# Performance work log

Hardware: AMD Instinct MI355X
Metric: run time of the kernel (lower is better)

Reference implementation:

```python
import jax, jax.numpy as jnp
import numpy as np

USER_COUNT = 100000
ITEM_COUNT = 50000
LATENT = 64
N_LAYERS = 3
NEG_SLOPE = 0.2


def _xavier(key, shape):
    fan_in, fan_out = shape[-2], shape[-1]
    lim = jnp.sqrt(6.0 / (fan_in + fan_out))
    return jax.random.uniform(key, shape, jnp.float32, -lim, lim)


def setup_inputs() -> dict:
    key = jax.random.key(0)
    ks = jax.random.split(key, 20)
    E = 2400000
    edge_index = jax.random.randint(ks[0], (2, E), 0, USER_COUNT + ITEM_COUNT, dtype=jnp.int64)
    user = jax.random.randint(ks[1], (4096,), 0, USER_COUNT, dtype=jnp.int64)
    item = jax.random.randint(ks[2], (4096,), 0, ITEM_COUNT, dtype=jnp.int64)
    inp = {"user": user, "item": item, "edge_index": edge_index}
    # online encoder params
    inp["user_emb_o"] = _xavier(ks[3], (USER_COUNT, LATENT))
    inp["item_emb_o"] = _xavier(ks[4], (ITEM_COUNT, LATENT))
    inp["W_o"] = _xavier(ks[5], (N_LAYERS, LATENT, LATENT))
    inp["att_src_o"] = _xavier(ks[6], (N_LAYERS, 1, LATENT))[:, 0, :]
    inp["att_dst_o"] = _xavier(ks[7], (N_LAYERS, 1, LATENT))[:, 0, :]
    inp["bias_o"] = jnp.zeros((N_LAYERS, LATENT), jnp.float32)
    # target encoder params (momentum copy; frozen in torch)
    inp["user_emb_t"] = _xavier(ks[8], (USER_COUNT, LATENT))
    inp["item_emb_t"] = _xavier(ks[9], (ITEM_COUNT, LATENT))
    inp["W_t"] = _xavier(ks[10], (N_LAYERS, LATENT, LATENT))
    inp["att_src_t"] = _xavier(ks[11], (N_LAYERS, 1, LATENT))[:, 0, :]
    inp["att_dst_t"] = _xavier(ks[12], (N_LAYERS, 1, LATENT))[:, 0, :]
    inp["bias_t"] = jnp.zeros((N_LAYERS, LATENT), jnp.float32)
    # predictor Linear(latent, latent)
    inp["pred_W"] = _xavier(ks[13], (LATENT, LATENT))
    inp["pred_b"] = jnp.zeros((LATENT,), jnp.float32)
    return inp


def _gat_conv(x, src, dst, n_nodes, W, a_src, a_dst, b):
    # PyG GATConv, heads=1, concat=True, add_self_loops handled by caller.
    h = x @ W                                   # [N, F]
    e = jax.nn.leaky_relu(jnp.take(h @ a_src, src) + jnp.take(h @ a_dst, dst), NEG_SLOPE)  # [E]
    m = jax.ops.segment_max(e, dst, num_segments=n_nodes)
    m = jnp.where(jnp.isfinite(m), m, 0.0)
    ex = jnp.exp(e - jnp.take(m, dst))
    den = jax.ops.segment_sum(ex, dst, num_segments=n_nodes)
    alpha = ex / jnp.take(den, dst)             # softmax over incoming edges per dst
    msg = alpha[:, None] * jnp.take(h, src, axis=0)  # [E, F]
    return jax.ops.segment_sum(msg, dst, num_segments=n_nodes) + b


def _encode(user_emb, item_emb, W, a_src, a_dst, bias, src, dst):
    x = jnp.concatenate([user_emb, item_emb], axis=0)  # [N, F]
    n_nodes = x.shape[0]
    for l in range(N_LAYERS):
        x = _gat_conv(x, src, dst, n_nodes, W[l], a_src[l], a_dst[l], bias[l])
    return x[:user_emb.shape[0]], x[user_emb.shape[0]:]


def reference(user_emb_o, item_emb_o, W_o, att_src_o, att_dst_o, bias_o,
              user_emb_t, item_emb_t, W_t, att_src_t, att_dst_t, bias_t,
              pred_W, pred_b, user, item, edge_index):
    n_nodes = user_emb_o.shape[0] + item_emb_o.shape[0]
    loops = jnp.arange(n_nodes, dtype=edge_index.dtype)
    src = jnp.concatenate([edge_index[0], loops])  # add self loops (PyG default)
    dst = jnp.concatenate([edge_index[1], loops])
    u_all_o, i_all_o = _encode(user_emb_o, item_emb_o, W_o, att_src_o, att_dst_o, bias_o, src, dst)
    u_all_t, i_all_t = _encode(user_emb_t, item_emb_t, W_t, att_src_t, att_dst_t, bias_t, src, dst)
    u_online = jnp.take(u_all_o, user, axis=0)
    i_online = jnp.take(i_all_o, item, axis=0)
    u_target = jnp.take(u_all_t, user, axis=0)
    i_target = jnp.take(i_all_t, item, axis=0)
    return (u_online @ pred_W.T + pred_b, u_target, i_online @ pred_W.T + pred_b, i_target)
```

## Files before the change

### kernel.cpp

```cpp
#include <hip/hip_runtime.h>
#include <math.h>
#include <stdint.h>

#define LAT 64
#define SLICE 16384

static inline int cdiv(int a, int b) { return (a + b - 1) / b; }

__global__ void k_count(const int* __restrict__ dst_arr, int E, int N, int* __restrict__ cnt) {
    int e = blockIdx.x * blockDim.x + threadIdx.x;
    int ET = E + N;
    if (e < ET) {
        int d = (e < E) ? dst_arr[e] : (e - E);
        atomicAdd(&cnt[d], 1);
    }
}

__global__ void k_scan1(const int* __restrict__ cnt, int N, int* __restrict__ out, int* __restrict__ blk_sums) {
    __shared__ int sdata[256];
    int t = threadIdx.x, b = blockIdx.x;
    int base = b * 1024 + t * 4;
    int v[4];
    int s = 0;
#pragma unroll
    for (int u = 0; u < 4; u++) { int i = base + u; v[u] = (i < N) ? cnt[i] : 0; s += v[u]; }
    sdata[t] = s; __syncthreads();
    for (int off = 1; off < 256; off <<= 1) {
        int x = (t >= off) ? sdata[t - off] : 0;
        __syncthreads();
        sdata[t] += x;
        __syncthreads();
    }
    int run = sdata[t] - s;
#pragma unroll
    for (int u = 0; u < 4; u++) { int i = base + u; if (i < N) out[i] = run; run += v[u]; }
    if (t == 255) blk_sums[b] = sdata[255];
}

__global__ void k_scan2(int* __restrict__ blk_sums, int NB) {
    __shared__ int sdata[256];
    int t = threadIdx.x;
    int v = (t < NB) ? blk_sums[t] : 0;
    sdata[t] = v; __syncthreads();
    for (int off = 1; off < 256; off <<= 1) {
        int x = (t >= off) ? sdata[t - off] : 0;
        __syncthreads();
        sdata[t] += x;
        __syncthreads();
    }
    if (t < NB) blk_sums[t] = sdata[t] - v;
}

__global__ void k_scan3(int* __restrict__ row_ptr, const int* __restrict__ blk_offs, int N, int ET) {
    int t = threadIdx.x, b = blockIdx.x;
    int base = b * 1024 + t * 4;
    int off = blk_offs[b];
#pragma unroll
    for (int u = 0; u < 4; u++) { int i = base + u; if (i < N) row_ptr[i] += off; }
    if (b == 0 && t == 0) row_ptr[N] = ET;
}

__global__ void k_scatter(const int* __restrict__ src_arr, const int* __restrict__ dst_arr, int E, int N,
                          const int* __restrict__ row_ptr, int* __restrict__ cnt, int* __restrict__ csr_src) {
    int ET = E + N;
    int slice = blockIdx.x >> 3;
    int range = blockIdx.x & 7;
    int rsz = (N + 7) >> 3;
    int lo = range * rsz;
    int hi = lo + rsz; if (hi > N) hi = N;
    int base = slice * SLICE;
    int end = base + SLICE; if (end > ET) end = ET;
    for (int e = base + threadIdx.x; e < end; e += 256) {
        int s, d;
        if (e < E) { s = src_arr[e]; d = dst_arr[e]; }
        else { s = e - E; d = e - E; }
        if (d >= lo && d < hi) {
            int pos = atomicAdd(&cnt[d], 1);
            csr_src[row_ptr[d] + pos] = s;
        }
    }
}


__global__ __launch_bounds__(256) void k_gemm2(const float* __restrict__ x,
                                               const float* __restrict__ ue, const float* __restrict__ ie, int NU,
                                               const float* __restrict__ W,
                                               const float* __restrict__ att_s, const float* __restrict__ att_d,
                                               float* __restrict__ h2e, float* __restrict__ asp, float* __restrict__ adp,
                                               int N) {
    __shared__ float sW[64 * 64];
    __shared__ float sX[128 * 65];
    __shared__ float sAs[64], sAd[64];
    int t = threadIdx.x;
    int row0 = blockIdx.x * 128;
    {
        const float4* Wv = (const float4*)W;
        float4* sWv = (float4*)sW;
#pragma unroll
        for (int u = 0; u < 4; u++) sWv[t + 256 * u] = Wv[t + 256 * u];
    }
    if (t < 64) { sAs[t] = att_s[t]; sAd[t] = att_d[t]; }
    {
#pragma unroll
        for (int u = 0; u < 8; u++) {
            int idx = t + 256 * u;
            int r = idx >> 4, c4 = idx & 15;
            int grow = row0 + r;
            float4 v = make_float4(0.f, 0.f, 0.f, 0.f);
            if (grow < N) {
                const float* base = x ? (x + (size_t)grow * 64)
                                      : (grow < NU ? ue + (size_t)grow * 64 : ie + (size_t)(grow - NU) * 64);
                v = ((const float4*)base)[c4];
            }
            int cc = c4 * 4;
            sX[r * 65 + cc] = v.x; sX[r * 65 + cc + 1] = v.y; sX[r * 65 + cc + 2] = v.z; sX[r * 65 + cc + 3] = v.w;
        }
    }
    __syncthreads();
    int rl = t >> 2;
    int g = t & 3;
    int c0 = g * 16;
    int rA = rl * 2, rB = rA + 1;
    float accA[16], accB[16];
#pragma unroll
    for (int j = 0; j < 16; j++) { accA[j] = 0.f; accB[j] = 0.f; }
    for (int k = 0; k < 64; k++) {
        float xa = sX[rA * 65 + k];
        float xb = sX[rB * 65 + k];
        const float4* wr = (const float4*)&sW[k * 64 + c0];
        float4 w0 = wr[0], w1 = wr[1], w2 = wr[2], w3 = wr[3];
        accA[0] += xa * w0.x; accA[1] += xa * w0.y; accA[2] += xa * w0.z; accA[3] += xa * w0.w;
        accA[4] += xa * w1.x; accA[5] += xa * w1.y; accA[6] += xa * w1.z; accA[7] += xa * w1.w;
        accA[8] += xa * w2.x; accA[9] += xa * w2.y; accA[10] += xa * w2.z; accA[11] += xa * w2.w;
        accA[12] += xa * w3.x; accA[13] += xa * w3.y; accA[14] += xa * w3.z; accA[15] += xa * w3.w;
        accB[0] += xb * w0.x; accB[1] += xb * w0.y; accB[2] += xb * w0.z; accB[3] += xb * w0.w;
        accB[4] += xb * w1.x; accB[5] += xb * w1.y; accB[6] += xb * w1.z; accB[7] += xb * w1.w;
        accB[8] += xb * w2.x; accB[9] += xb * w2.y; accB[10] += xb * w2.z; accB[11] += xb * w2.w;
        accB[12] += xb * w3.x; accB[13] += xb * w3.y; accB[14] += xb * w3.z; accB[15] += xb * w3.w;
    }
    float sA = 0.f, dA = 0.f, sB = 0.f, dB = 0.f;
#pragma unroll
    for (int j = 0; j < 16; j++) {
        sA += accA[j] * sAs[c0 + j]; dA += accA[j] * sAd[c0 + j];
        sB += accB[j] * sAs[c0 + j]; dB += accB[j] * sAd[c0 + j];
    }
    sA += __shfl_xor(sA, 1); sA += __shfl_xor(sA, 2);
    dA += __shfl_xor(dA, 1); dA += __shfl_xor(dA, 2);
    sB += __shfl_xor(sB, 1); sB += __shfl_xor(sB, 2);
    dB += __shfl_xor(dB, 1); dB += __shfl_xor(dB, 2);
    int rowA = row0 + rA, rowB = row0 + rB;
    if (rowA < N) {
        if (g == 0) { asp[(size_t)rowA * 2] = sA; adp[(size_t)rowA * 2] = dA; }
        float4* hv = (float4*)&h2e[(size_t)rowA * 128 + c0];
        hv[0] = make_float4(accA[0], accA[1], accA[2], accA[3]);
        hv[1] = make_float4(accA[4], accA[5], accA[6], accA[7]);
        hv[2] = make_float4(accA[8], accA[9], accA[10], accA[11]);
        hv[3] = make_float4(accA[12], accA[13], accA[14], accA[15]);
    }
    if (rowB < N) {
        if (g == 0) { asp[(size_t)rowB * 2] = sB; adp[(size_t)rowB * 2] = dB; }
        float4* hv = (float4*)&h2e[(size_t)rowB * 128 + c0];
        hv[0] = make_float4(accB[0], accB[1], accB[2], accB[3]);
        hv[1] = make_float4(accB[4], accB[5], accB[6], accB[7]);
        hv[2] = make_float4(accB[8], accB[9], accB[10], accB[11]);
        hv[3] = make_float4(accB[12], accB[13], accB[14], accB[15]);
    }
}

__global__ __launch_bounds__(256) void k_agg2(const float* __restrict__ h2,
                                              const int* __restrict__ row_ptr, const int* __restrict__ csr_src,
                                              const float2* __restrict__ asv, const float2* __restrict__ adv,
                                              const float* __restrict__ bias_o, const float* __restrict__ bias_t,
                                              float* __restrict__ xo, float* __restrict__ xt, int N,
                                              const int* __restrict__ selu, const int* __restrict__ seli,
                                              int nSel, int nSelU, int NU,
                                              float* __restrict__ selxo, float* __restrict__ outT_u,
                                              float* __restrict__ outT_i) {
    int wid = threadIdx.x >> 6, lane = threadIdx.x & 63;
    int r = blockIdx.x * 4 + wid;
    int d;
    float *po, *pt;
    if (selu) {
        if (r >= nSel) return;
        if (r < nSelU) { d = selu[r]; pt = outT_u + (size_t)r * 64; }
        else { int rr = r - nSelU; d = seli[rr] + NU; pt = outT_i + (size_t)rr * 64; }
        po = selxo + (size_t)r * 64;
    } else {
        if (r >= N) return;
        d = r;
        po = xo + (size_t)d * 64;
        pt = xt + (size_t)d * 64;
    }
    int s0 = row_ptr[d], s1 = row_ptr[d + 1];
    float2 advv = adv[d];
    int j0 = s0 + lane;
    int sv0 = 0; float eo0 = -1e30f, et0 = -1e30f;
    if (j0 < s1) {
        sv0 = csr_src[j0];
        float2 a2 = asv[sv0];
        float eo = a2.x + advv.x; eo0 = (eo > 0.f) ? eo : 0.2f * eo;
        float et = a2.y + advv.y; et0 = (et > 0.f) ? et : 0.2f * et;
    }
    float mo = eo0, mt = et0;
    for (int j = j0 + 64; j < s1; j += 64) {
        float2 a2 = asv[csr_src[j]];
        float eo = a2.x + advv.x; eo = (eo > 0.f) ? eo : 0.2f * eo; mo = fmaxf(mo, eo);
        float et = a2.y + advv.y; et = (et > 0.f) ? et : 0.2f * et; mt = fmaxf(mt, et);
    }
#pragma unroll
    for (int o = 32; o; o >>= 1) { mo = fmaxf(mo, __shfl_xor(mo, o)); mt = fmaxf(mt, __shfl_xor(mt, o)); }
    float exo0 = (j0 < s1) ? expf(eo0 - mo) : 0.f;
    float ext0 = (j0 < s1) ? expf(et0 - mt) : 0.f;
    float so = exo0, st = ext0;
    for (int j = j0 + 64; j < s1; j += 64) {
        float2 a2 = asv[csr_src[j]];
        float eo = a2.x + advv.x; eo = (eo > 0.f) ? eo : 0.2f * eo; so += expf(eo - mo);
        float et = a2.y + advv.y; et = (et > 0.f) ? et : 0.2f * et; st += expf(et - mt);
    }
#pragma unroll
    for (int o = 32; o; o >>= 1) { so += __shfl_xor(so, o); st += __shfl_xor(st, o); }
    float invo = 1.f / so, invt = 1.f / st;
    exo0 *= invo; ext0 *= invt;
    int sub = lane >> 4, c4 = lane & 15;
    float4 ao = make_float4(0.f, 0.f, 0.f, 0.f);
    float4 at4 = make_float4(0.f, 0.f, 0.f, 0.f);
    for (int cb = s0; cb < s1; cb += 64) {
        int sv; float wo, wt;
        if (cb == s0) { sv = sv0; wo = exo0; wt = ext0; }
        else {
            int jj = cb + lane; sv = 0; wo = 0.f; wt = 0.f;
            if (jj < s1) {
                sv = csr_src[jj];
                float2 a2 = asv[sv];
                float eo = a2.x + advv.x; eo = (eo > 0.f) ? eo : 0.2f * eo; wo = expf(eo - mo) * invo;
                float et = a2.y + advv.y; et = (et > 0.f) ? et : 0.2f * et; wt = expf(et - mt) * invt;
            }
        }
        int c = s1 - cb; if (c > 64) c = 64;
        for (int q = 0; q < c; q += 4) {
            int il = q + sub;
            int s = __shfl(sv, il);
            float o_ = __shfl(wo, il);
            float t_ = __shfl(wt, il);
            const float* hb = h2 + (size_t)s * 128 + (c4 << 2);
            float4 ho = *(const float4*)hb;
            float4 ht = *(const float4*)(hb + 64);
            ao.x += o_ * ho.x; ao.y += o_ * ho.y; ao.z += o_ * ho.z; ao.w += o_ * ho.w;
            at4.x += t_ * ht.x; at4.y += t_ * ht.y; at4.z += t_ * ht.z; at4.w += t_ * ht.w;
        }
    }
#pragma unroll
    for (int o = 16; o <= 32; o <<= 1) {
        ao.x += __shfl_xor(ao.x, o); ao.y += __shfl_xor(ao.y, o);
        ao.z += __shfl_xor(ao.z, o); ao.w += __shfl_xor(ao.w, o);
        at4.x += __shfl_xor(at4.x, o); at4.y += __shfl_xor(at4.y, o);
        at4.z += __shfl_xor(at4.z, o); at4.w += __shfl_xor(at4.w, o);
    }
    if (lane < 16) {
        float4 bo = ((const float4*)bias_o)[c4];
        ao.x += bo.x; ao.y += bo.y; ao.z += bo.z; ao.w += bo.w;
        ((float4*)po)[c4] = ao;
        float4 bt = ((const float4*)bias_t)[c4];
        at4.x += bt.x; at4.y += bt.y; at4.z += bt.z; at4.w += bt.w;
        ((float4*)pt)[c4] = at4;
    }
}

__global__ __launch_bounds__(256) void k_gemm(const float* __restrict__ x,
                                              const float* __restrict__ ue, const float* __restrict__ ie, int NU,
                                              const float* __restrict__ W,
                                              const float* __restrict__ att_s, const float* __restrict__ att_d,
                                              float* __restrict__ h, float* __restrict__ as_, float* __restrict__ ad_,
                                              int N) {
    __shared__ float sW[64 * 64];
    __shared__ float sX[128 * 65];
    __shared__ float sAs[64], sAd[64];
    int t = threadIdx.x;
    int row0 = blockIdx.x * 128;
    {
        const float4* Wv = (const float4*)W;
        float4* sWv = (float4*)sW;
#pragma unroll
        for (int u = 0; u < 4; u++) sWv[t + 256 * u] = Wv[t + 256 * u];
    }
    if (t < 64) { sAs[t] = att_s[t]; sAd[t] = att_d[t]; }
    {
#pragma unroll
        for (int u = 0; u < 8; u++) {
            int idx = t + 256 * u;
            int r = idx >> 4, c4 = idx & 15;
            int grow = row0 + r;
            float4 v = make_float4(0.f, 0.f, 0.f, 0.f);
            if (grow < N) {
                const float* base = x ? (x + (size_t)grow * 64)
                                      : (grow < NU ? ue + (size_t)grow * 64 : ie + (size_t)(grow - NU) * 64);
                v = ((const float4*)base)[c4];
            }
            int cc = c4 * 4;
            sX[r * 65 + cc] = v.x; sX[r * 65 + cc + 1] = v.y; sX[r * 65 + cc + 2] = v.z; sX[r * 65 + cc + 3] = v.w;
        }
    }
    __syncthreads();
    int rl = t >> 2;
    int g = t & 3;
    int c0 = g * 16;
    int rA = rl * 2, rB = rA + 1;
    float accA[16], accB[16];
#pragma unroll
    for (int j = 0; j < 16; j++) { accA[j] = 0.f; accB[j] = 0.f; }
    for (int k = 0; k < 64; k++) {
        float xa = sX[rA * 65 + k];
        float xb = sX[rB * 65 + k];
        const float4* wr = (const float4*)&sW[k * 64 + c0];
        float4 w0 = wr[0], w1 = wr[1], w2 = wr[2], w3 = wr[3];
        accA[0] += xa * w0.x; accA[1] += xa * w0.y; accA[2] += xa * w0.z; accA[3] += xa * w0.w;
        accA[4] += xa * w1.x; accA[5] += xa * w1.y; accA[6] += xa * w1.z; accA[7] += xa * w1.w;
        accA[8] += xa * w2.x; accA[9] += xa * w2.y; accA[10] += xa * w2.z; accA[11] += xa * w2.w;
        accA[12] += xa * w3.x; accA[13] += xa * w3.y; accA[14] += xa * w3.z; accA[15] += xa * w3.w;
        accB[0] += xb * w0.x; accB[1] += xb * w0.y; accB[2] += xb * w0.z; accB[3] += xb * w0.w;
        accB[4] += xb * w1.x; accB[5] += xb * w1.y; accB[6] += xb * w1.z; accB[7] += xb * w1.w;
        accB[8] += xb * w2.x; accB[9] += xb * w2.y; accB[10] += xb * w2.z; accB[11] += xb * w2.w;
        accB[12] += xb * w3.x; accB[13] += xb * w3.y; accB[14] += xb * w3.z; accB[15] += xb * w3.w;
    }
    float sA = 0.f, dA = 0.f, sB = 0.f, dB = 0.f;
#pragma unroll
    for (int j = 0; j < 16; j++) {
        sA += accA[j] * sAs[c0 + j]; dA += accA[j] * sAd[c0 + j];
        sB += accB[j] * sAs[c0 + j]; dB += accB[j] * sAd[c0 + j];
    }
    sA += __shfl_xor(sA, 1); sA += __shfl_xor(sA, 2);
    dA += __shfl_xor(dA, 1); dA += __shfl_xor(dA, 2);
    sB += __shfl_xor(sB, 1); sB += __shfl_xor(sB, 2);
    dB += __shfl_xor(dB, 1); dB += __shfl_xor(dB, 2);
    int rowA = row0 + rA, rowB = row0 + rB;
    if (rowA < N) {
        if (g == 0) { as_[rowA] = sA; ad_[rowA] = dA; }
        float4* hv = (float4*)&h[(size_t)rowA * 64 + c0];
        hv[0] = make_float4(accA[0], accA[1], accA[2], accA[3]);
        hv[1] = make_float4(accA[4], accA[5], accA[6], accA[7]);
        hv[2] = make_float4(accA[8], accA[9], accA[10], accA[11]);
        hv[3] = make_float4(accA[12], accA[13], accA[14], accA[15]);
    }
    if (rowB < N) {
        if (g == 0) { as_[rowB] = sB; ad_[rowB] = dB; }
        float4* hv = (float4*)&h[(size_t)rowB * 64 + c0];
        hv[0] = make_float4(accB[0], accB[1], accB[2], accB[3]);
        hv[1] = make_float4(accB[4], accB[5], accB[6], accB[7]);
        hv[2] = make_float4(accB[8], accB[9], accB[10], accB[11]);
        hv[3] = make_float4(accB[12], accB[13], accB[14], accB[15]);
    }
}

__global__ __launch_bounds__(256) void k_agg(const float* __restrict__ h,
                                             const int* __restrict__ row_ptr, const int* __restrict__ csr_src,
                                             const float* __restrict__ as_, const float* __restrict__ ad_,
                                             const float* __restrict__ bias, float* __restrict__ xout, int N) {
    int wid = threadIdx.x >> 6, lane = threadIdx.x & 63;
    int d = blockIdx.x * 4 + wid;
    if (d >= N) return;
    int s0 = row_ptr[d], s1 = row_ptr[d + 1];
    float adv = ad_[d];
    int j0 = s0 + lane;
    int sv0 = 0; float ev0 = -1e30f;
    if (j0 < s1) {
        sv0 = csr_src[j0];
        float e = as_[sv0] + adv;
        ev0 = (e > 0.f) ? e : 0.2f * e;
    }
    float m = ev0;
    for (int j = j0 + 64; j < s1; j += 64) {
        float e = as_[csr_src[j]] + adv;
        e = (e > 0.f) ? e : 0.2f * e;
        m = fmaxf(m, e);
    }
#pragma unroll
    for (int o = 32; o; o >>= 1) m = fmaxf(m, __shfl_xor(m, o));
    float ex0 = (j0 < s1) ? expf(ev0 - m) : 0.f;
    float sum = ex0;
    for (int j = j0 + 64; j < s1; j += 64) {
        float e = as_[csr_src[j]] + adv;
        e = (e > 0.f) ? e : 0.2f * e;
        sum += expf(e - m);
    }
#pragma unroll
    for (int o = 32; o; o >>= 1) sum += __shfl_xor(sum, o);
    float inv = 1.f / sum;
    ex0 *= inv;
    int sub = lane >> 4;
    int c4 = lane & 15;
    float4 acc = make_float4(0.f, 0.f, 0.f, 0.f);
    for (int cbase = s0; cbase < s1; cbase += 64) {
        int sv; float ex;
        if (cbase == s0) { sv = sv0; ex = ex0; }
        else {
            int jj = cbase + lane;
            sv = 0; ex = 0.f;
            if (jj < s1) {
                sv = csr_src[jj];
                float e = as_[sv] + adv;
                e = (e > 0.f) ? e : 0.2f * e;
                ex = expf(e - m) * inv;
            }
        }
        int cnt2 = s1 - cbase; if (cnt2 > 64) cnt2 = 64;
        for (int q = 0; q < cnt2; q += 4) {
            int il = q + sub;
            float w = __shfl(ex, il);
            int s = __shfl(sv, il);
            const float4 hv = *(const float4*)&h[(size_t)s * 64 + (c4 << 2)];
            acc.x += w * hv.x; acc.y += w * hv.y; acc.z += w * hv.z; acc.w += w * hv.w;
        }
    }
#pragma unroll
    for (int o = 16; o <= 32; o <<= 1) {
        acc.x += __shfl_xor(acc.x, o);
        acc.y += __shfl_xor(acc.y, o);
        acc.z += __shfl_xor(acc.z, o);
        acc.w += __shfl_xor(acc.w, o);
    }
    if (lane < 16) {
        float4 bv = ((const float4*)bias)[c4];
        acc.x += bv.x; acc.y += bv.y; acc.z += bv.z; acc.w += bv.w;
        ((float4*)&xout[(size_t)d * 64])[c4] = acc;
    }
}

__global__ __launch_bounds__(256) void k_pred(const float* __restrict__ x, const int* __restrict__ idx,
                                              int nIdx, int rowOff, const float* __restrict__ W,
                                              const float* __restrict__ bvec, float* __restrict__ out) {
    __shared__ float sWt[64 * 65];
    int t = threadIdx.x;
#pragma unroll
    for (int u = 0; u < 16; u++) {
        int i = u * 256 + t;
        int c = i >> 6, k = i & 63;
        sWt[k * 65 + c] = W[i];
    }
    __syncthreads();
    int wid = t >> 6, lane = t & 63;
    int r = blockIdx.x * 4 + wid;
    if (r >= nIdx) return;
    int node = idx ? (idx[r] + rowOff) : (r + rowOff);
    float xr = x[(size_t)node * 64 + lane];
    float acc = bvec[lane];
    for (int k = 0; k < 64; k++)
        acc += __shfl(xr, k) * sWt[k * 65 + lane];
    out[(size_t)r * 64 + lane] = acc;
}

__global__ void k_gather(const float* __restrict__ x, const int* __restrict__ idx, int nIdx, int rowOff,
                         float* __restrict__ out) {
    int t = blockIdx.x * blockDim.x + threadIdx.x;
    if (t < nIdx * 64) {
        int r = t >> 6, c = t & 63;
        int node = idx[r] + rowOff;
        out[t] = x[(size_t)node * 64 + c];
    }
}

extern "C" void kernel_launch(void* const* d_in, const int* in_sizes, int n_in,
                              void* d_out, int out_size, void* d_ws, size_t ws_size,
                              hipStream_t stream) {
    const int* user = (const int*)d_in[0];
    const int* item = (const int*)d_in[1];
    const int* edge = (const int*)d_in[2];
    const float* user_emb_o = (const float*)d_in[3];
    const float* item_emb_o = (const float*)d_in[4];
    const float* W_o = (const float*)d_in[5];
    const float* att_src_o = (const float*)d_in[6];
    const float* att_dst_o = (const float*)d_in[7];
    const float* bias_o = (const float*)d_in[8];
    const float* user_emb_t = (const float*)d_in[9];
    const float* item_emb_t = (const float*)d_in[10];
    const float* W_t = (const float*)d_in[11];
    const float* att_src_t = (const float*)d_in[12];
    const float* att_dst_t = (const float*)d_in[13];
    const float* bias_t = (const float*)d_in[14];
    const float* pred_W = (const float*)d_in[15];
    const float* pred_b = (const float*)d_in[16];
    float* out = (float*)d_out;

    int E = in_sizes[2] / 2;
    int NU = in_sizes[3] / LAT;
    int NI = in_sizes[4] / LAT;
    int N = NU + NI;
    int ET = E + N;
    int nU = in_sizes[0];
    int nI = in_sizes[1];
    int nSel = nU + nI;

    const int* src_arr = edge;
    const int* dst_arr = edge + E;

    auto al = [](size_t v) { return (v + 255) & ~(size_t)255; };

    char* p = (char*)d_ws;
    float* x_o   = (float*)p;  p += al((size_t)N * LAT * 4);
    float* x_t   = (float*)p;  p += al((size_t)N * LAT * 4);
    float* h2    = (float*)p;  p += al((size_t)N * 2 * LAT * 4);
    float2* asv  = (float2*)p; p += al((size_t)N * 8);
    float2* adv  = (float2*)p; p += al((size_t)N * 8);
    int* row_ptr = (int*)p;    p += al((size_t)(N + 1) * 4);
    int* cnt     = (int*)p;    p += al((size_t)N * 4);
    int* csr_src = (int*)p;    p += al((size_t)ET * 4);
    int* blk     = (int*)p;    p += al(4096);
    float* xsel  = (float*)p;  p += al((size_t)nSel * LAT * 4);
    size_t need_primary = (size_t)(p - (char*)d_ws);

    bool primary = ws_size >= need_primary;

    if (primary) {
        hipMemsetAsync(cnt, 0, (size_t)N * 4, stream);
        k_count<<<cdiv(ET, 256), 256, 0, stream>>>(dst_arr, E, N, cnt);
        int NB = cdiv(N, 1024);
        k_scan1<<<NB, 256, 0, stream>>>(cnt, N, row_ptr, blk);
        k_scan2<<<1, 256, 0, stream>>>(blk, NB);
        k_scan3<<<NB, 256, 0, stream>>>(row_ptr, blk, N, ET);
        hipMemsetAsync(cnt, 0, (size_t)N * 4, stream);
        k_scatter<<<cdiv(ET, SLICE) * 8, 256, 0, stream>>>(src_arr, dst_arr, E, N, row_ptr, cnt, csr_src);

        for (int l = 0; l < 3; l++) {
            const float* xo_in = (l == 0) ? nullptr : x_o;
            const float* xt_in = (l == 0) ? nullptr : x_t;
            k_gemm2<<<cdiv(N, 128), 256, 0, stream>>>(xo_in, user_emb_o, item_emb_o, NU,
                                                      W_o + l * 64 * 64, att_src_o + l * 64, att_dst_o + l * 64,
                                                      h2, (float*)asv, (float*)adv, N);
            k_gemm2<<<cdiv(N, 128), 256, 0, stream>>>(xt_in, user_emb_t, item_emb_t, NU,
                                                      W_t + l * 64 * 64, att_src_t + l * 64, att_dst_t + l * 64,
                                                      h2 + 64, (float*)asv + 1, (float*)adv + 1, N);
            if (l < 2) {
                k_agg2<<<cdiv(N, 4), 256, 0, stream>>>(h2, row_ptr, csr_src, asv, adv,
                                                       bias_o + l * 64, bias_t + l * 64,
                                                       x_o, x_t, N,
                                                       nullptr, nullptr, 0, 0, NU, nullptr, nullptr, nullptr);
            } else {
                k_agg2<<<cdiv(nSel, 4), 256, 0, stream>>>(h2, row_ptr, csr_src, asv, adv,
                                                          bias_o + l * 64, bias_t + l * 64,
                                                          nullptr, nullptr, N,
                                                          user, item, nSel, nU, NU,
                                                          xsel, out + (size_t)nU * LAT,
                                                          out + (size_t)3 * nU * LAT);
            }
        }
        k_pred<<<cdiv(nU, 4), 256, 0, stream>>>(xsel, nullptr, nU, 0, pred_W, pred_b, out);
        k_pred<<<cdiv(nI, 4), 256, 0, stream>>>(xsel, nullptr, nI, nU, pred_W, pred_b,
                                                out + (size_t)2 * nU * LAT);
        return;
    }

    p = (char*)d_ws;
    float* x_cur = (float*)p;  p += al((size_t)N * LAT * 4);
    float* h     = (float*)p;  p += al((size_t)N * LAT * 4);
    float* as_   = (float*)p;  p += al((size_t)N * 4);
    float* ad_   = (float*)p;  p += al((size_t)N * 4);
    row_ptr = (int*)p;         p += al((size_t)(N + 1) * 4);
    cnt     = (int*)p;         p += al((size_t)N * 4);
    csr_src = (int*)p;         p += al((size_t)ET * 4);
    blk     = (int*)p;         p += al(4096);

    hipMemsetAsync(cnt, 0, (size_t)N * 4, stream);
    k_count<<<cdiv(ET, 256), 256, 0, stream>>>(dst_arr, E, N, cnt);
    int NB = cdiv(N, 1024);
    k_scan1<<<NB, 256, 0, stream>>>(cnt, N, row_ptr, blk);
    k_scan2<<<1, 256, 0, stream>>>(blk, NB);
    k_scan3<<<NB, 256, 0, stream>>>(row_ptr, blk, N, ET);
    hipMemsetAsync(cnt, 0, (size_t)N * 4, stream);
    k_scatter<<<cdiv(ET, SLICE) * 8, 256, 0, stream>>>(src_arr, dst_arr, E, N, row_ptr, cnt, csr_src);

    auto run_encoder = [&](const float* ue, const float* ie, const float* Wl,
                           const float* asl, const float* adl, const float* bl) {
        for (int l = 0; l < 3; l++) {
            const float* xin = (l == 0) ? nullptr : x_cur;
            k_gemm<<<cdiv(N, 128), 256, 0, stream>>>(xin, ue, ie, NU, Wl + l * 64 * 64, asl + l * 64,
                                                     adl + l * 64, h, as_, ad_, N);
            k_agg<<<cdiv(N, 4), 256, 0, stream>>>(h, row_ptr, csr_src, as_, ad_, bl + l * 64, x_cur, N);
        }
    };

    run_encoder(user_emb_o, item_emb_o, W_o, att_src_o, att_dst_o, bias_o);
    k_pred<<<cdiv(nU, 4), 256, 0, stream>>>(x_cur, user, nU, 0, pred_W, pred_b, out);
    k_pred<<<cdiv(nI, 4), 256, 0, stream>>>(x_cur, item, nI, NU, pred_W, pred_b, out + (size_t)2 * nU * LAT);

    run_encoder(user_emb_t, item_emb_t, W_t, att_src_t, att_dst_t, bias_t);
    k_gather<<<cdiv(nU * LAT, 256), 256, 0, stream>>>(x_cur, user, nU, 0, out + (size_t)nU * LAT);
    k_gather<<<cdiv(nI * LAT, 256), 256, 0, stream>>>(x_cur, item, nI, NU, out + (size_t)3 * nU * LAT);
}
```

Measured before the change: 856.9 us.

## Fuse GAT aggregation with next-layer linear transform and attention projections

Adds a persistent kernel that, for each destination node, computes the edge softmax, aggregates neighbor features, adds bias, and immediately multiplies by the next layer's weight matrix held in shared memory. It also produces the next layer's source and destination attention scalars. This removes the intermediate x_o/x_t write and re-read and the separate GEMM launches for layers 1 and 2, using ping-pong h2 buffers. The tradeoff is that each wave does a 64x64 matvec through shuffles, and the aggregation now uses one float4 per lane with 4 edges in parallel. That may differ in efficiency from the old k_agg2, and the fixed grid of 4096 blocks may under- or over-subscribe the GPU.

```diff
diff --git a/kernel.cpp b/kernel.cpp
--- a/kernel.cpp
+++ b/kernel.cpp
@@ -164,6 +164,110 @@
         hv[1] = make_float4(accB[4], accB[5], accB[6], accB[7]);
         hv[2] = make_float4(accB[8], accB[9], accB[10], accB[11]);
         hv[3] = make_float4(accB[12], accB[13], accB[14], accB[15]);
+    }
+}
+
+__global__ __launch_bounds__(256) void k_fused(const float* __restrict__ h2_in,
+        const int* __restrict__ row_ptr, const int* __restrict__ csr_src,
+        const float* __restrict__ asv_in, const float* __restrict__ adv_in,
+        const float* __restrict__ bias_o, const float* __restrict__ bias_t,
+        const float* __restrict__ Wn_o, const float* __restrict__ Wn_t,
+        const float* __restrict__ attsn_o, const float* __restrict__ attdn_o,
+        const float* __restrict__ attsn_t, const float* __restrict__ attdn_t,
+        float* __restrict__ h2_out, float* __restrict__ asv_out, float* __restrict__ adv_out,
+        int N) {
+    __shared__ float sW[64 * 65];
+    int enc = blockIdx.x & 1;
+    int bb = blockIdx.x >> 1;
+    int t = threadIdx.x;
+    const float* Wn = enc ? Wn_t : Wn_o;
+#pragma unroll
+    for (int u = 0; u < 16; u++) {
+        int i = u * 256 + t;
+        int k = i >> 6, c = i & 63;
+        sW[c * 65 + k] = Wn[i];
+    }
+    __syncthreads();
+    int wid = t >> 6, lane = t & 63;
+    float attSv = (enc ? attsn_t : attsn_o)[lane];
+    float attDv = (enc ? attdn_t : attdn_o)[lane];
+    int c4 = lane & 15, sub = lane >> 4;
+    float4 bias4 = ((const float4*)(enc ? bias_t : bias_o))[c4];
+    int nWaves = (gridDim.x >> 1) * 4;
+    for (int d = bb * 4 + wid; d < N; d += nWaves) {
+        int s0 = row_ptr[d], s1 = row_ptr[d + 1];
+        float advv = adv_in[(size_t)d * 2 + enc];
+        int j0 = s0 + lane;
+        int sv0 = 0; float ev0 = -1e30f;
+        if (j0 < s1) {
+            sv0 = csr_src[j0];
+            float e = asv_in[(size_t)sv0 * 2 + enc] + advv;
+            ev0 = (e > 0.f) ? e : 0.2f * e;
+        }
+        float m = ev0;
+        for (int j = j0 + 64; j < s1; j += 64) {
+            float e = asv_in[(size_t)csr_src[j] * 2 + enc] + advv;
+            e = (e > 0.f) ? e : 0.2f * e;
+            m = fmaxf(m, e);
+        }
+#pragma unroll
+        for (int o = 32; o; o >>= 1) m = fmaxf(m, __shfl_xor(m, o));
+        float ex0 = (j0 < s1) ? expf(ev0 - m) : 0.f;
+        float sum = ex0;
+        for (int j = j0 + 64; j < s1; j += 64) {
+            float e = asv_in[(size_t)csr_src[j] * 2 + enc] + advv;
+            e = (e > 0.f) ? e : 0.2f * e;
+            sum += expf(e - m);
+        }
+#pragma unroll
+        for (int o = 32; o; o >>= 1) sum += __shfl_xor(sum, o);
+        float inv = 1.f / sum;
+        ex0 *= inv;
+        float4 acc = make_float4(0.f, 0.f, 0.f, 0.f);
+        for (int cb = s0; cb < s1; cb += 64) {
+            int sv; float ex;
+            if (cb == s0) { sv = sv0; ex = ex0; }
+            else {
+                int jj = cb + lane; sv = 0; ex = 0.f;
+                if (jj < s1) {
+                    sv = csr_src[jj];
+                    float e = asv_in[(size_t)sv * 2 + enc] + advv;
+                    e = (e > 0.f) ? e : 0.2f * e;
+                    ex = expf(e - m) * inv;
+                }
+            }
+            int c = s1 - cb; if (c > 64) c = 64;
+            for (int q = 0; q < c; q += 4) {
+                int il = q + sub;
+                int s = __shfl(sv, il);
+                float w = __shfl(ex, il);
+                const float4 hv = *(const float4*)&h2_in[(size_t)s * 128 + enc * 64 + (c4 << 2)];
+                acc.x += w * hv.x; acc.y += w * hv.y; acc.z += w * hv.z; acc.w += w * hv.w;
+            }
+        }
+#pragma unroll
+        for (int o = 16; o <= 32; o <<= 1) {
+            acc.x += __shfl_xor(acc.x, o); acc.y += __shfl_xor(acc.y, o);
+            acc.z += __shfl_xor(acc.z, o); acc.w += __shfl_xor(acc.w, o);
+        }
+        float4 xr;
+        xr.x = acc.x + bias4.x; xr.y = acc.y + bias4.y;
+        xr.z = acc.z + bias4.z; xr.w = acc.w + bias4.w;
+        float hacc = 0.f;
+#pragma unroll
+        for (int k4 = 0; k4 < 16; k4++) {
+            const float4 wv = *(const float4*)&sW[lane * 65 + k4 * 4];
+            hacc += __shfl(xr.x, k4) * wv.x + __shfl(xr.y, k4) * wv.y +
+                    __shfl(xr.z, k4) * wv.z + __shfl(xr.w, k4) * wv.w;
+        }
+        float so = hacc * attSv, sd = hacc * attDv;
+#pragma unroll
+        for (int o = 32; o; o >>= 1) { so += __shfl_xor(so, o); sd += __shfl_xor(sd, o); }
+        h2_out[(size_t)d * 128 + enc * 64 + lane] = hacc;
+        if (lane == 0) {
+            asv_out[(size_t)d * 2 + enc] = so;
+            adv_out[(size_t)d * 2 + enc] = sd;
+        }
     }
 }
 
@@ -495,11 +599,12 @@
     auto al = [](size_t v) { return (v + 255) & ~(size_t)255; };
 
     char* p = (char*)d_ws;
-    float* x_o   = (float*)p;  p += al((size_t)N * LAT * 4);
-    float* x_t   = (float*)p;  p += al((size_t)N * LAT * 4);
-    float* h2    = (float*)p;  p += al((size_t)N * 2 * LAT * 4);
-    float2* asv  = (float2*)p; p += al((size_t)N * 8);
-    float2* adv  = (float2*)p; p += al((size_t)N * 8);
+    float* h2a   = (float*)p;  p += al((size_t)N * 2 * LAT * 4);
+    float* h2b   = (float*)p;  p += al((size_t)N * 2 * LAT * 4);
+    float* asa   = (float*)p;  p += al((size_t)N * 8);
+    float* ada   = (float*)p;  p += al((size_t)N * 8);
+    float* asb   = (float*)p;  p += al((size_t)N * 8);
+    float* adb   = (float*)p;  p += al((size_t)N * 8);
     int* row_ptr = (int*)p;    p += al((size_t)(N + 1) * 4);
     int* cnt     = (int*)p;    p += al((size_t)N * 4);
     int* csr_src = (int*)p;    p += al((size_t)ET * 4);
@@ -519,29 +624,30 @@
         hipMemsetAsync(cnt, 0, (size_t)N * 4, stream);
         k_scatter<<<cdiv(ET, SLICE) * 8, 256, 0, stream>>>(src_arr, dst_arr, E, N, row_ptr, cnt, csr_src);
 
-        for (int l = 0; l < 3; l++) {
-            const float* xo_in = (l == 0) ? nullptr : x_o;
-            const float* xt_in = (l == 0) ? nullptr : x_t;
-            k_gemm2<<<cdiv(N, 128), 256, 0, stream>>>(xo_in, user_emb_o, item_emb_o, NU,
-                                                      W_o + l * 64 * 64, att_src_o + l * 64, att_dst_o + l * 64,
-                                                      h2, (float*)asv, (float*)adv, N);
-            k_gemm2<<<cdiv(N, 128), 256, 0, stream>>>(xt_in, user_emb_t, item_emb_t, NU,
-                                                      W_t + l * 64 * 64, att_src_t + l * 64, att_dst_t + l * 64,
-                                                      h2 + 64, (float*)asv + 1, (float*)adv + 1, N);
-            if (l < 2) {
-                k_agg2<<<cdiv(N, 4), 256, 0, stream>>>(h2, row_ptr, csr_src, asv, adv,
-                                                       bias_o + l * 64, bias_t + l * 64,
-                                                       x_o, x_t, N,
-                                                       nullptr, nullptr, 0, 0, NU, nullptr, nullptr, nullptr);
-            } else {
-                k_agg2<<<cdiv(nSel, 4), 256, 0, stream>>>(h2, row_ptr, csr_src, asv, adv,
-                                                          bias_o + l * 64, bias_t + l * 64,
-                                                          nullptr, nullptr, N,
-                                                          user, item, nSel, nU, NU,
-                                                          xsel, out + (size_t)nU * LAT,
-                                                          out + (size_t)3 * nU * LAT);
-            }
-        }
+        k_gemm2<<<cdiv(N, 128), 256, 0, stream>>>(nullptr, user_emb_o, item_emb_o, NU,
+                                                  W_o, att_src_o, att_dst_o,
+                                                  h2a, asa, ada, N);
+        k_gemm2<<<cdiv(N, 128), 256, 0, stream>>>(nullptr, user_emb_t, item_emb_t, NU,
+                                                  W_t, att_src_t, att_dst_t,
+                                                  h2a + 64, asa + 1, ada + 1, N);
+        k_fused<<<4096, 256, 0, stream>>>(h2a, row_ptr, csr_src, asa, ada,
+                                          bias_o, bias_t,
+                                          W_o + 4096, W_t + 4096,
+                                          att_src_o + 64, att_dst_o + 64,
+                                          att_src_t + 64, att_dst_t + 64,
+                                          h2b, asb, adb, N);
+        k_fused<<<4096, 256, 0, stream>>>(h2b, row_ptr, csr_src, asb, adb,
+                                          bias_o + 64, bias_t + 64,
+                                          W_o + 2 * 4096, W_t + 2 * 4096,
+                                          att_src_o + 128, att_dst_o + 128,
+                                          att_src_t + 128, att_dst_t + 128,
+                                          h2a, asa, ada, N);
+        k_agg2<<<cdiv(nSel, 4), 256, 0, stream>>>(h2a, row_ptr, csr_src, (const float2*)asa, (const float2*)ada,
+                                                  bias_o + 128, bias_t + 128,
+                                                  nullptr, nullptr, N,
+                                                  user, item, nSel, nU, NU,
+                                                  xsel, out + (size_t)nU * LAT,
+                                                  out + (size_t)3 * nU * LAT);
         k_pred<<<cdiv(nU, 4), 256, 0, stream>>>(xsel, nullptr, nU, 0, pred_W, pred_b, out);
         k_pred<<<cdiv(nI, 4), 256, 0, stream>>>(xsel, nullptr, nI, nU, pred_W, pred_b,
                                                 out + (size_t)2 * nU * LAT);
```

Result: slower. 1.270 ms (+48.1%).

## Bin edges by destination range before CSR scatter, merge dual-encoder GEMMs, unroll aggregation

Applied to the files above, without the earlier changes.

CSR construction now uses a two-pass binning scheme. The first pass counts degrees and writes (src,dst) pairs into eight destination-range buckets, using x_o as scratch. The second pass scatters each bucket into csr_src. This replaces the old scatter, which re-read the whole edge list eight times and filtered by range. The two per-layer encoder GEMM launches are merged into one launch that picks the encoder by block parity, and the aggregation inner loop is unrolled to process two neighbors per step. The cost is extra bucket storage traffic and an added dependency on scratch sizing (bcap).

```diff
diff --git a/kernel.cpp b/kernel.cpp
--- a/kernel.cpp
+++ b/kernel.cpp
@@ -4,17 +4,9 @@
 
 #define LAT 64
 #define SLICE 16384
+#define BIN_CHUNK 1024
 
 static inline int cdiv(int a, int b) { return (a + b - 1) / b; }
-
-__global__ void k_count(const int* __restrict__ dst_arr, int E, int N, int* __restrict__ cnt) {
-    int e = blockIdx.x * blockDim.x + threadIdx.x;
-    int ET = E + N;
-    if (e < ET) {
-        int d = (e < E) ? dst_arr[e] : (e - E);
-        atomicAdd(&cnt[d], 1);
-    }
-}
 
 __global__ void k_scan1(const int* __restrict__ cnt, int N, int* __restrict__ out, int* __restrict__ blk_sums) {
     __shared__ int sdata[256];
@@ -58,6 +50,74 @@
 #pragma unroll
     for (int u = 0; u < 4; u++) { int i = base + u; if (i < N) row_ptr[i] += off; }
     if (b == 0 && t == 0) row_ptr[N] = ET;
+}
+
+__global__ __launch_bounds__(256) void k_binA(const int* __restrict__ src_arr, const int* __restrict__ dst_arr,
+                                              int E, int N, int ET, int rsz, int bcap,
+                                              int2* __restrict__ buckets, int* __restrict__ gcur,
+                                              int* __restrict__ cnt) {
+    __shared__ int lcnt[8], lbase[8];
+    int t = threadIdx.x;
+    for (int base = blockIdx.x * BIN_CHUNK; base < ET; base += gridDim.x * BIN_CHUNK) {
+        if (t < 8) lcnt[t] = 0;
+        __syncthreads();
+        int s[4], d[4], r[4], lofs[4];
+        int nval = 0;
+        if (base + BIN_CHUNK <= E) {
+            int4 s4 = ((const int4*)(src_arr + base))[t];
+            int4 d4 = ((const int4*)(dst_arr + base))[t];
+            s[0] = s4.x; s[1] = s4.y; s[2] = s4.z; s[3] = s4.w;
+            d[0] = d4.x; d[1] = d4.y; d[2] = d4.z; d[3] = d4.w;
+            nval = 4;
+        } else {
+            for (int k = 0; k < 4; k++) {
+                int e = base + t * 4 + k;
+                if (e < ET) {
+                    if (e < E) { s[nval] = src_arr[e]; d[nval] = dst_arr[e]; }
+                    else { s[nval] = e - E; d[nval] = e - E; }
+                    nval++;
+                }
+            }
+        }
+        for (int k = 0; k < nval; k++) {
+            r[k] = d[k] / rsz;
+            lofs[k] = atomicAdd(&lcnt[r[k]], 1);
+            atomicAdd(&cnt[d[k]], 1);
+        }
+        __syncthreads();
+        if (t < 8) lbase[t] = atomicAdd(&gcur[t], lcnt[t]);
+        __syncthreads();
+        for (int k = 0; k < nval; k++) {
+            buckets[(size_t)r[k] * bcap + lbase[r[k]] + lofs[k]] = make_int2(s[k], d[k]);
+        }
+        __syncthreads();
+    }
+}
+
+__global__ __launch_bounds__(256) void k_binB(const int2* __restrict__ buckets, int bcap,
+                                              const int* __restrict__ gcur,
+                                              const int* __restrict__ row_ptr, int* __restrict__ cnt,
+                                              int* __restrict__ csr_src) {
+    int r = blockIdx.x & 7;
+    int nb = blockIdx.x >> 3;
+    int stride = (gridDim.x >> 3) * 256;
+    int total = gcur[r];
+    const int* bp = (const int*)(buckets + (size_t)r * bcap);
+    for (int i = nb * 256 + threadIdx.x; i < total; i += stride) {
+        int s = __builtin_nontemporal_load(bp + 2 * i);
+        int d = __builtin_nontemporal_load(bp + 2 * i + 1);
+        int pos = atomicAdd(&cnt[d], 1);
+        csr_src[row_ptr[d] + pos] = s;
+    }
+}
+
+__global__ void k_count(const int* __restrict__ dst_arr, int E, int N, int* __restrict__ cnt) {
+    int e = blockIdx.x * blockDim.x + threadIdx.x;
+    int ET = E + N;
+    if (e < ET) {
+        int d = (e < E) ? dst_arr[e] : (e - E);
+        atomicAdd(&cnt[d], 1);
+    }
 }
 
 __global__ void k_scatter(const int* __restrict__ src_arr, const int* __restrict__ dst_arr, int E, int N,
@@ -81,18 +141,27 @@
     }
 }
 
-
-__global__ __launch_bounds__(256) void k_gemm2(const float* __restrict__ x,
-                                               const float* __restrict__ ue, const float* __restrict__ ie, int NU,
-                                               const float* __restrict__ W,
-                                               const float* __restrict__ att_s, const float* __restrict__ att_d,
-                                               float* __restrict__ h2e, float* __restrict__ asp, float* __restrict__ adp,
-                                               int N) {
+__global__ __launch_bounds__(256) void k_gemm2m(const float* __restrict__ xo, const float* __restrict__ xt,
+        const float* __restrict__ ueo, const float* __restrict__ ieo,
+        const float* __restrict__ uet, const float* __restrict__ iet, int NU,
+        const float* __restrict__ Wo, const float* __restrict__ Wt,
+        const float* __restrict__ atso, const float* __restrict__ atdo,
+        const float* __restrict__ atst, const float* __restrict__ atdt,
+        float* __restrict__ h2, float* __restrict__ asp, float* __restrict__ adp, int N) {
     __shared__ float sW[64 * 64];
     __shared__ float sX[128 * 65];
     __shared__ float sAs[64], sAd[64];
+    int enc = blockIdx.x & 1;
+    int bb = blockIdx.x >> 1;
+    const float* x = enc ? xt : xo;
+    const float* ue = enc ? uet : ueo;
+    const float* ie = enc ? iet : ieo;
+    const float* W = enc ? Wt : Wo;
+    const float* att_s = enc ? atst : atso;
+    const float* att_d = enc ? atdt : atdo;
+    float* h2e = h2 + enc * 64;
     int t = threadIdx.x;
-    int row0 = blockIdx.x * 128;
+    int row0 = bb * 128;
     {
         const float4* Wv = (const float4*)W;
         float4* sWv = (float4*)sW;
@@ -150,7 +219,7 @@
     dB += __shfl_xor(dB, 1); dB += __shfl_xor(dB, 2);
     int rowA = row0 + rA, rowB = row0 + rB;
     if (rowA < N) {
-        if (g == 0) { asp[(size_t)rowA * 2] = sA; adp[(size_t)rowA * 2] = dA; }
+        if (g == 0) { asp[(size_t)rowA * 2 + enc] = sA; adp[(size_t)rowA * 2 + enc] = dA; }
         float4* hv = (float4*)&h2e[(size_t)rowA * 128 + c0];
         hv[0] = make_float4(accA[0], accA[1], accA[2], accA[3]);
         hv[1] = make_float4(accA[4], accA[5], accA[6], accA[7]);
@@ -158,7 +227,7 @@
         hv[3] = make_float4(accA[12], accA[13], accA[14], accA[15]);
     }
     if (rowB < N) {
-        if (g == 0) { asp[(size_t)rowB * 2] = sB; adp[(size_t)rowB * 2] = dB; }
+        if (g == 0) { asp[(size_t)rowB * 2 + enc] = sB; adp[(size_t)rowB * 2 + enc] = dB; }
         float4* hv = (float4*)&h2e[(size_t)rowB * 128 + c0];
         hv[0] = make_float4(accB[0], accB[1], accB[2], accB[3]);
         hv[1] = make_float4(accB[4], accB[5], accB[6], accB[7]);
@@ -237,7 +306,24 @@
             }
         }
         int c = s1 - cb; if (c > 64) c = 64;
-        for (int q = 0; q < c; q += 4) {
+        int q = 0;
+        for (; q + 8 <= c; q += 8) {
+            int ilA = q + sub, ilB = q + 4 + sub;
+            int sA = __shfl(sv, ilA), sB = __shfl(sv, ilB);
+            float oA = __shfl(wo, ilA), oB = __shfl(wo, ilB);
+            float tA = __shfl(wt, ilA), tB = __shfl(wt, ilB);
+            const float* ha = h2 + (size_t)sA * 128 + (c4 << 2);
+            const float* hb = h2 + (size_t)sB * 128 + (c4 << 2);
+            float4 hoA = *(const float4*)ha;
+            float4 htA = *(const float4*)(ha + 64);
+            float4 hoB = *(const float4*)hb;
+            float4 htB = *(const float4*)(hb + 64);
+            ao.x += oA * hoA.x; ao.y += oA * hoA.y; ao.z += oA * hoA.z; ao.w += oA * hoA.w;
+            at4.x += tA * htA.x; at4.y += tA * htA.y; at4.z += tA * htA.z; at4.w += tA * htA.w;
+            ao.x += oB * hoB.x; ao.y += oB * hoB.y; ao.z += oB * hoB.z; ao.w += oB * hoB.w;
+            at4.x += tB * htB.x; at4.y += tB * htB.y; at4.z += tB * htB.z; at4.w += tB * htB.w;
+        }
+        for (; q < c; q += 4) {
             int il = q + sub;
             int s = __shfl(sv, il);
             float o_ = __shfl(wo, il);
@@ -488,6 +574,7 @@
     int nU = in_sizes[0];
     int nI = in_sizes[1];
     int nSel = nU + nI;
+    int rsz = (N + 7) >> 3;
 
     const int* src_arr = edge;
     const int* dst_arr = edge + E;
@@ -498,48 +585,54 @@
     float* x_o   = (float*)p;  p += al((size_t)N * LAT * 4);
     float* x_t   = (float*)p;  p += al((size_t)N * LAT * 4);
     float* h2    = (float*)p;  p += al((size_t)N * 2 * LAT * 4);
-    float2* asv  = (float2*)p; p += al((size_t)N * 8);
-    float2* adv  = (float2*)p; p += al((size_t)N * 8);
+    float* asv   = (float*)p;  p += al((size_t)N * 8);
+    float* adv   = (float*)p;  p += al((size_t)N * 8);
     int* row_ptr = (int*)p;    p += al((size_t)(N + 1) * 4);
     int* cnt     = (int*)p;    p += al((size_t)N * 4);
     int* csr_src = (int*)p;    p += al((size_t)ET * 4);
     int* blk     = (int*)p;    p += al(4096);
+    int* gcur    = (int*)p;    p += al(64);
     float* xsel  = (float*)p;  p += al((size_t)nSel * LAT * 4);
     size_t need_primary = (size_t)(p - (char*)d_ws);
 
+    int bcap = ET / 8 + 16384;
+    int2* buckets = (int2*)x_o;
+
     bool primary = ws_size >= need_primary;
 
     if (primary) {
         hipMemsetAsync(cnt, 0, (size_t)N * 4, stream);
-        k_count<<<cdiv(ET, 256), 256, 0, stream>>>(dst_arr, E, N, cnt);
+        hipMemsetAsync(gcur, 0, 32, stream);
+        k_binA<<<1024, 256, 0, stream>>>(src_arr, dst_arr, E, N, ET, rsz, bcap, buckets, gcur, cnt);
         int NB = cdiv(N, 1024);
         k_scan1<<<NB, 256, 0, stream>>>(cnt, N, row_ptr, blk);
         k_scan2<<<1, 256, 0, stream>>>(blk, NB);
         k_scan3<<<NB, 256, 0, stream>>>(row_ptr, blk, N, ET);
         hipMemsetAsync(cnt, 0, (size_t)N * 4, stream);
-        k_scatter<<<cdiv(ET, SLICE) * 8, 256, 0, stream>>>(src_arr, dst_arr, E, N, row_ptr, cnt, csr_src);
+        k_binB<<<1024, 256, 0, stream>>>(buckets, bcap, gcur, row_ptr, cnt, csr_src);
 
         for (int l = 0; l < 3; l++) {
             const float* xo_in = (l == 0) ? nullptr : x_o;
             const float* xt_in = (l == 0) ? nullptr : x_t;
-            k_gemm2<<<cdiv(N, 128), 256, 0, stream>>>(xo_in, user_emb_o, item_emb_o, NU,
-                                                      W_o + l * 64 * 64, att_src_o + l * 64, att_dst_o + l * 64,
-                                                      h2, (float*)asv, (float*)adv, N);
-            k_gemm2<<<cdiv(N, 128), 256, 0, stream>>>(xt_in, user_emb_t, item_emb_t, NU,
-                                                      W_t + l * 64 * 64, att_src_t + l * 64, att_dst_t + l * 64,
-                                                      h2 + 64, (float*)asv + 1, (float*)adv + 1, N);
+            k_gemm2m<<<cdiv(N, 128) * 2, 256, 0, stream>>>(xo_in, xt_in,
+                    user_emb_o, item_emb_o, user_emb_t, item_emb_t, NU,
+                    W_o + l * 4096, W_t + l * 4096,
+                    att_src_o + l * 64, att_dst_o + l * 64,
+                    att_src_t + l * 64, att_dst_t + l * 64,
+                    h2, asv, adv, N);
             if (l < 2) {
-                k_agg2<<<cdiv(N, 4), 256, 0, stream>>>(h2, row_ptr, csr_src, asv, adv,
-                                                       bias_o + l * 64, bias_t + l * 64,
-                                                       x_o, x_t, N,
-                                                       nullptr, nullptr, 0, 0, NU, nullptr, nullptr, nullptr);
+                k_agg2<<<cdiv(N, 4), 256, 0, stream>>>(h2, row_ptr, csr_src,
+                        (const float2*)asv, (const float2*)adv,
+                        bias_o + l * 64, bias_t + l * 64,
+                        x_o, x_t, N,
+                        nullptr, nullptr, 0, 0, NU, nullptr, nullptr, nullptr);
             } else {
-                k_agg2<<<cdiv(nSel, 4), 256, 0, stream>>>(h2, row_ptr, csr_src, asv, adv,
-                                                          bias_o + l * 64, bias_t + l * 64,
-                                                          nullptr, nullptr, N,
-                                                          user, item, nSel, nU, NU,
-                                                          xsel, out + (size_t)nU * LAT,
-                                                          out + (size_t)3 * nU * LAT);
+                k_agg2<<<cdiv(nSel, 4), 256, 0, stream>>>(h2, row_ptr, csr_src,
+                        (const float2*)asv, (const float2*)adv,
+                        bias_o + l * 64, bias_t + l * 64,
+                        nullptr, nullptr, N,
+                        user, item, nSel, nU, NU,
+                        xsel, out + (size_t)nU * LAT, out + (size_t)3 * nU * LAT);
             }
         }
         k_pred<<<cdiv(nU, 4), 256, 0, stream>>>(xsel, nullptr, nU, 0, pred_W, pred_b, out);
```

New measurement: 847.5 us. About the same (-1.1%).
